# Optimization experiments

Hardware: AMD Instinct MI355X
Metric: run time of the kernel (lower is better)

Reference implementation:

```python
import jax, jax.numpy as jnp
import numpy as np

D, H, W, C = 24, 24, 16, 2        # image_dims + num_classes
THETA_ALPHA = 160.0               # bilateral spatial std
THETA_BETA = 3.0                  # bilateral intensity std
THETA_GAMMA = 3.0                 # spatial-only std
NUM_ITERATIONS = 5
N = D * H * W


def _gauss_kernel(feats):
    # Dense Gaussian kernel K_ij = exp(-0.5 * ||f_i - f_j||^2).
    # This is the exact filter that the permutohedral lattice approximates
    # (self-term included, matching the lattice splat/blur/slice behaviour).
    sq = jnp.sum(feats * feats, axis=-1)               # [N]
    d2 = sq[:, None] + sq[None, :] - 2.0 * feats @ feats.T
    return jnp.exp(-0.5 * jnp.maximum(d2, 0.0))        # [N, N]


def _positions():
    zz, yy, xx = jnp.meshgrid(jnp.arange(D), jnp.arange(H), jnp.arange(W), indexing='ij')
    return jnp.stack([zz, yy, xx], axis=-1).reshape(N, 3).astype(jnp.float32)


def setup_inputs() -> dict:
    key = jax.random.key(0)
    k1, k2 = jax.random.split(key)
    unaries = jax.random.normal(k1, (1, D, H, W, C), dtype=jnp.float32)
    rgb = jax.random.uniform(k2, (1, D, H, W, 1), dtype=jnp.float32)
    # learned params (build() initial values)
    spatial_ker_weights = jnp.array([1.41, 1.41], dtype=jnp.float32)
    bilateral_ker_weights = jnp.array([3.85, 3.85], dtype=jnp.float32)
    compatibility_matrix = jnp.eye(C, dtype=jnp.float32)
    return dict(unaries=unaries, rgb=rgb,
                spatial_ker_weights=spatial_ker_weights,
                bilateral_ker_weights=bilateral_ker_weights,
                compatibility_matrix=compatibility_matrix)


def reference(unaries, rgb, spatial_ker_weights, bilateral_ker_weights, compatibility_matrix):
    out_shape = unaries.shape
    u = unaries.reshape(N, C)                 # batch index 0 only, as in the TF code
    img = rgb.reshape(N, -1)
    pos = _positions()

    Ks = _gauss_kernel(pos / THETA_GAMMA)                                        # spatial kernel [N,N]
    Kb = _gauss_kernel(jnp.concatenate([pos / THETA_ALPHA, img / THETA_BETA], -1))  # bilateral kernel [N,N]

    # normalization = filter applied to all-ones (row sums)
    norm_s = jnp.sum(Ks, axis=-1, keepdims=True)   # [N,1]
    norm_b = jnp.sum(Kb, axis=-1, keepdims=True)   # [N,1]

    q = u
    for _ in range(NUM_ITERATIONS):
        spatial_out = (Ks @ q) / norm_s            # [N,C]
        bilateral_out = (Kb @ q) / norm_b          # [N,C]
        # diag(w_s) @ spatial.T + diag(w_b) @ bilateral.T  ==  per-class scaling
        message = spatial_out * spatial_ker_weights + bilateral_out * bilateral_ker_weights
        pairwise = message @ compatibility_matrix.T  # (compat @ msg.T).T
        q = u - pairwise
    return q.reshape(out_shape)
```

## Files before the change

kernel.cpp:

```cpp
#include <hip/hip_runtime.h>


#define DD 24
#define HH 24
#define WW 16
#define SLICE 384
#define NPTS 9216
#define NT 5
#define NPAIR 6
#define NPTOT 9
#define LOG2E 1.4426950408889634f
#define K3L   (LOG2E / 18.0f)
#define K160L (LOG2E / 51200.0f)
#define EXP2  __builtin_amdgcn_exp2f

static __device__ __forceinline__ int iabs(int a) { return a < 0 ? -a : a; }

__global__ __launch_bounds__(SLICE)
void k_pre(const float2* __restrict__ u2, const float* __restrict__ rgb,
           float2* __restrict__ tmp2, float* __restrict__ normS) {
    __shared__ float gk[32];
    __shared__ float2 sA[HH][WW + 1];
    __shared__ float2 sB[HH][WW + 1];
    const int z = blockIdx.x, p = blockIdx.y, t = threadIdx.x;
    const int y = t >> 4, x = t & 15;
    const int i = z * SLICE + t;

    const float kk = (p == 0) ? K3L : K160L;
    if (t < DD) gk[t] = EXP2(-(float)(t * t) * kk);

    const float I3 = rgb[i] * (1.f / 3.f);
    float Pt[NT];
    Pt[0] = EXP2(-0.5f * LOG2E * I3 * I3);
#pragma unroll
    for (int k = 1; k < NT; ++k) Pt[k] = Pt[k - 1] * I3;

    float2 v;
    if (p == 0) {
        v = u2[i];
    } else if (p < NPAIR) {
        float2 q = u2[i];
        float P = Pt[p - 1];
        v = make_float2(P * q.x, P * q.y);
    } else {
        int j = p - NPAIR;
        v = make_float2(Pt[2 * j], (j < 2) ? Pt[2 * j + 1] : 0.f);
    }
    sA[y][x] = v;
    __syncthreads();

    float a0 = 0.f, a1 = 0.f;
#pragma unroll
    for (int xp = 0; xp < WW; ++xp) {
        float w = gk[iabs(x - xp)];
        float2 vv = sA[y][xp];
        a0 = fmaf(w, vv.x, a0);
        a1 = fmaf(w, vv.y, a1);
    }
    sB[y][x] = make_float2(a0, a1);
    __syncthreads();
    float b0 = 0.f, b1 = 0.f;
#pragma unroll
    for (int yp = 0; yp < HH; ++yp) {
        float w = gk[iabs(y - yp)];
        float2 vv = sB[yp][x];
        b0 = fmaf(w, vv.x, b0);
        b1 = fmaf(w, vv.y, b1);
    }
    tmp2[p * NPTS + i] = make_float2(b0, b1);

    if (p == 0) {
        float sx = 0.f, sy = 0.f, sz = 0.f;
#pragma unroll
        for (int xp = 0; xp < WW; ++xp) sx += gk[iabs(x - xp)];
#pragma unroll
        for (int yp = 0; yp < HH; ++yp) sy += gk[iabs(y - yp)];
#pragma unroll
        for (int zp = 0; zp < DD; ++zp) sz += gk[iabs(z - zp)];
        normS[i] = 1.0f / (sx * sy * sz);
    }
}

__global__ __launch_bounds__(SLICE)
void k_zconv(const float2* __restrict__ tmp2, float2* __restrict__ zout2) {
    const int z = blockIdx.x, p = blockIdx.y, t = threadIdx.x;
    const float kk = (p == 0) ? K3L : K160L;
    float acc0 = 0.f, acc1 = 0.f;
    const float2* src = tmp2 + p * NPTS + t;
#pragma unroll 6
    for (int zp = 0; zp < DD; ++zp) {
        int d = z - zp;
        float w = EXP2(-(float)(d * d) * kk);
        float2 v = src[zp * SLICE];
        acc0 = fmaf(w, v.x, acc0);
        acc1 = fmaf(w, v.y, acc1);
    }
    zout2[p * NPTS + z * SLICE + t] = make_float2(acc0, acc1);
}

static __device__ __forceinline__ void mf_update(
        const float2 zp_[NPAIR], const float* Pt, float inv_ns, float inv_nb,
        const float* sw, const float* bw, const float* compat,
        const float2 uu, float* q0o, float* q1o) {
    const float invf[NT] = {1.f, 1.f, 0.5f, 1.f / 6.f, 1.f / 24.f};
    float b0 = 0.f, b1 = 0.f;
#pragma unroll
    for (int k = 0; k < NT; ++k) {
        float w = Pt[k] * invf[k];
        b0 = fmaf(w, zp_[1 + k].x, b0);
        b1 = fmaf(w, zp_[1 + k].y, b1);
    }
    b0 *= inv_nb;
    b1 *= inv_nb;
    float s0 = zp_[0].x * inv_ns;
    float s1 = zp_[0].y * inv_ns;
    float m0 = s0 * sw[0] + b0 * bw[0];
    float m1 = s1 * sw[1] + b1 * bw[1];
    float p0 = fmaf(compat[0], m0, compat[1] * m1);
    float p1 = fmaf(compat[2], m0, compat[3] * m1);
    *q0o = uu.x - p0;
    *q1o = uu.y - p1;
}

__global__ __launch_bounds__(SLICE)
void k_xyupd(const float2* __restrict__ zout2, const float* __restrict__ rgb,
             const float2* __restrict__ u2,
             const float* __restrict__ sw, const float* __restrict__ bw,
             const float* __restrict__ compat,
             const float* __restrict__ normS, float* __restrict__ normB,
             float2* __restrict__ tmp2, int it) {
    __shared__ float gk[32];
    __shared__ float2 sA[HH][WW + 1];
    __shared__ float2 sB[HH][WW + 1];
    const int z = blockIdx.x, p = blockIdx.y, t = threadIdx.x;
    const int y = t >> 4, x = t & 15;
    const int i = z * SLICE + t;

    const float kk = (p == 0) ? K3L : K160L;
    if (t < DD) gk[t] = EXP2(-(float)(t * t) * kk);

    float2 zp_[NPAIR];
#pragma unroll
    for (int k = 0; k < NPAIR; ++k) zp_[k] = zout2[k * NPTS + i];

    const float I3 = rgb[i] * (1.f / 3.f);
    float Pt[NT];
    Pt[0] = EXP2(-0.5f * LOG2E * I3 * I3);
#pragma unroll
    for (int k = 1; k < NT; ++k) Pt[k] = Pt[k - 1] * I3;

    float inv_nb;
    if (it == 0) {
        float2 n0 = zout2[6 * NPTS + i];
        float2 n1 = zout2[7 * NPTS + i];
        float2 n2 = zout2[8 * NPTS + i];
        float nb = Pt[0] * n0.x + Pt[1] * n0.y + 0.5f * Pt[2] * n1.x
                 + (1.f / 6.f) * Pt[3] * n1.y + (1.f / 24.f) * Pt[4] * n2.x;
        if (p == 0) normB[i] = nb;
        inv_nb = 1.0f / nb;
    } else {
        inv_nb = 1.0f / normB[i];
    }

    float q0, q1;
    mf_update(zp_, Pt, normS[i], inv_nb, sw, bw, compat, u2[i], &q0, &q1);

    float2 v;
    if (p == 0) v = make_float2(q0, q1);
    else { float P = Pt[p - 1]; v = make_float2(P * q0, P * q1); }

    sA[y][x] = v;
    __syncthreads();
    float a0 = 0.f, a1 = 0.f;
#pragma unroll
    for (int xp = 0; xp < WW; ++xp) {
        float w = gk[iabs(x - xp)];
        float2 vv = sA[y][xp];
        a0 = fmaf(w, vv.x, a0);
        a1 = fmaf(w, vv.y, a1);
    }
    sB[y][x] = make_float2(a0, a1);
    __syncthreads();
    float b0 = 0.f, b1 = 0.f;
#pragma unroll
    for (int yp = 0; yp < HH; ++yp) {
        float w = gk[iabs(y - yp)];
        float2 vv = sB[yp][x];
        b0 = fmaf(w, vv.x, b0);
        b1 = fmaf(w, vv.y, b1);
    }
    tmp2[p * NPTS + i] = make_float2(b0, b1);
}

__global__ __launch_bounds__(256)
void k_final(const float2* __restrict__ zout2, const float* __restrict__ rgb,
             const float2* __restrict__ u2,
             const float* __restrict__ sw, const float* __restrict__ bw,
             const float* __restrict__ compat,
             const float* __restrict__ normS, const float* __restrict__ normB,
             float2* __restrict__ out) {
    const int i = blockIdx.x * 256 + threadIdx.x;

    float2 zp_[NPAIR];
#pragma unroll
    for (int k = 0; k < NPAIR; ++k) zp_[k] = zout2[k * NPTS + i];

    const float I3 = rgb[i] * (1.f / 3.f);
    float Pt[NT];
    Pt[0] = EXP2(-0.5f * LOG2E * I3 * I3);
#pragma unroll
    for (int k = 1; k < NT; ++k) Pt[k] = Pt[k - 1] * I3;

    float q0, q1;
    mf_update(zp_, Pt, normS[i], 1.0f / normB[i], sw, bw, compat,
              u2[i], &q0, &q1);
    out[i] = make_float2(q0, q1);
}

extern "C" void kernel_launch(void* const* d_in, const int* in_sizes, int n_in,
                              void* d_out, int out_size, void* d_ws, size_t ws_size,
                              hipStream_t stream) {
    const float2* u2     = (const float2*)d_in[0];
    const float*  rgb    = (const float*)d_in[1];
    const float*  sw     = (const float*)d_in[2];
    const float*  bw     = (const float*)d_in[3];
    const float*  compat = (const float*)d_in[4];
    float2* out = (float2*)d_out;

    float2* ws2   = (float2*)d_ws;
    float2* tmp2  = ws2;
    float2* zout2 = ws2 + NPTOT * NPTS;
    float*  normS = (float*)(ws2 + 2 * NPTOT * NPTS);
    float*  normB = normS + NPTS;

    k_pre<<<dim3(DD, NPTOT), SLICE, 0, stream>>>(u2, rgb, tmp2, normS);

    for (int it = 0; it < 5; ++it) {
        k_zconv<<<dim3(DD, it == 0 ? NPTOT : NPAIR), SLICE, 0, stream>>>(tmp2, zout2);
        if (it < 4)
            k_xyupd<<<dim3(DD, NPAIR), SLICE, 0, stream>>>(zout2, rgb, u2, sw, bw,
                                                           compat, normS, normB,
                                                           tmp2, it);
        else
            k_final<<<NPTS / 256, 256, 0, stream>>>(zout2, rgb, u2, sw, bw,
                                                    compat, normS, normB, out);
    }
}
```

Measured before the change: 97.98 us.

## Fuse full 3D separable convolution per channel into one block with atomic message accumulation

Each of the pairing channels is now processed by a single 512-thread block that holds the whole 24x24x16 volume in LDS and runs the x, y and z passes in place, replacing the separate xy and z kernels. The mean-field update is split so that each channel block atomically adds its weighted contribution into a per-iteration message buffer, which the next iteration or the final kernel reads. This cuts the kernel launch count and global round trips. The cost is that only 6-9 blocks run on a GPU with many CUs, the two float components are filtered in sequence, and float atomics make the summation order nondeterministic.

```diff
diff --git a/kernel.cpp b/kernel.cpp
--- a/kernel.cpp
+++ b/kernel.cpp
@@ -4,217 +4,308 @@
 #define DD 24
 #define HH 24
 #define WW 16
-#define SLICE 384
+#define XS 17
+#define YSTR (HH * XS)
 #define NPTS 9216
+#define NBLK 512
+#define PPT 18
 #define NT 5
-#define NPAIR 6
-#define NPTOT 9
 #define LOG2E 1.4426950408889634f
 #define K3L   (LOG2E / 18.0f)
 #define K160L (LOG2E / 51200.0f)
 #define EXP2  __builtin_amdgcn_exp2f
 
-static __device__ __forceinline__ int iabs(int a) { return a < 0 ? -a : a; }
-
-__global__ __launch_bounds__(SLICE)
+#define LIDX(i) (XS * ((i) >> 4) + ((i) & 15))
+
+static __device__ __forceinline__ void pass_x(float* A, const float* w, int t) {
+    float i0[WW], o0[WW], i1[WW], o1[WW];
+    const int b0 = XS * t;
+    const int b1 = XS * (NBLK + t);
+    const bool two = (t < (DD * HH - NBLK));
+#pragma unroll
+    for (int xp = 0; xp < WW; ++xp) i0[xp] = A[b0 + xp];
+    if (two) {
+#pragma unroll
+        for (int xp = 0; xp < WW; ++xp) i1[xp] = A[b1 + xp];
+    }
+#pragma unroll
+    for (int x = 0; x < WW; ++x) {
+        float a = 0.f;
+#pragma unroll
+        for (int xp = 0; xp < WW; ++xp)
+            a = fmaf(w[x > xp ? x - xp : xp - x], i0[xp], a);
+        o0[x] = a;
+    }
+    if (two) {
+#pragma unroll
+        for (int x = 0; x < WW; ++x) {
+            float a = 0.f;
+#pragma unroll
+            for (int xp = 0; xp < WW; ++xp)
+                a = fmaf(w[x > xp ? x - xp : xp - x], i1[xp], a);
+            o1[x] = a;
+        }
+    }
+    __syncthreads();
+#pragma unroll
+    for (int x = 0; x < WW; ++x) A[b0 + x] = o0[x];
+    if (two) {
+#pragma unroll
+        for (int x = 0; x < WW; ++x) A[b1 + x] = o1[x];
+    }
+    __syncthreads();
+}
+
+static __device__ __forceinline__ void pass_y(float* A, const float* w, int t) {
+    float in[HH], o[HH];
+    const bool act = (t < DD * WW);
+    const int base = (t >> 4) * YSTR + (t & 15);
+    if (act) {
+#pragma unroll
+        for (int yp = 0; yp < HH; ++yp) in[yp] = A[base + XS * yp];
+#pragma unroll
+        for (int y = 0; y < HH; ++y) {
+            float a = 0.f;
+#pragma unroll
+            for (int yp = 0; yp < HH; ++yp)
+                a = fmaf(w[y > yp ? y - yp : yp - y], in[yp], a);
+            o[y] = a;
+        }
+    }
+    __syncthreads();
+    if (act) {
+#pragma unroll
+        for (int y = 0; y < HH; ++y) A[base + XS * y] = o[y];
+    }
+    __syncthreads();
+}
+
+static __device__ __forceinline__ void pass_z(float* A, const float* w, int t) {
+    float in[DD], o[DD];
+    const bool act = (t < HH * WW);
+    const int base = (t >> 4) * XS + (t & 15);
+    if (act) {
+#pragma unroll
+        for (int zp = 0; zp < DD; ++zp) in[zp] = A[base + YSTR * zp];
+#pragma unroll
+        for (int z = 0; z < DD; ++z) {
+            float a = 0.f;
+#pragma unroll
+            for (int zp = 0; zp < DD; ++zp)
+                a = fmaf(w[z > zp ? z - zp : zp - z], in[zp], a);
+            o[z] = a;
+        }
+    }
+    __syncthreads();
+    if (act) {
+#pragma unroll
+        for (int z = 0; z < DD; ++z) A[base + YSTR * z] = o[z];
+    }
+    __syncthreads();
+}
+
+static __device__ __forceinline__ void conv3(float* A, const float* w, int t) {
+    pass_x(A, w, t);
+    pass_y(A, w, t);
+    pass_z(A, w, t);
+}
+
+__global__ __launch_bounds__(NBLK, 2)
 void k_pre(const float2* __restrict__ u2, const float* __restrict__ rgb,
-           float2* __restrict__ tmp2, float* __restrict__ normS) {
-    __shared__ float gk[32];
-    __shared__ float2 sA[HH][WW + 1];
-    __shared__ float2 sB[HH][WW + 1];
-    const int z = blockIdx.x, p = blockIdx.y, t = threadIdx.x;
-    const int y = t >> 4, x = t & 15;
-    const int i = z * SLICE + t;
-
+           float2* __restrict__ zout, float* __restrict__ normS,
+           float2* __restrict__ msgAll) {
+    __shared__ float A[DD * YSTR];
+    __shared__ float sxl[WW], syl[HH], szl[DD];
+    const int p = blockIdx.x, t = threadIdx.x;
     const float kk = (p == 0) ? K3L : K160L;
-    if (t < DD) gk[t] = EXP2(-(float)(t * t) * kk);
-
-    const float I3 = rgb[i] * (1.f / 3.f);
-    float Pt[NT];
-    Pt[0] = EXP2(-0.5f * LOG2E * I3 * I3);
-#pragma unroll
-    for (int k = 1; k < NT; ++k) Pt[k] = Pt[k - 1] * I3;
-
-    float2 v;
+
+    float w[24];
+#pragma unroll
+    for (int d = 0; d < 24; ++d) w[d] = EXP2(-(float)(d * d) * kk);
+
+    {
+        int g = p * NBLK + t;
+        for (int j = g; j < 4 * NPTS; j += 9 * NBLK)
+            msgAll[j] = make_float2(0.f, 0.f);
+    }
+
     if (p == 0) {
-        v = u2[i];
-    } else if (p < NPAIR) {
-        float2 q = u2[i];
-        float P = Pt[p - 1];
-        v = make_float2(P * q.x, P * q.y);
-    } else {
-        int j = p - NPAIR;
-        v = make_float2(Pt[2 * j], (j < 2) ? Pt[2 * j + 1] : 0.f);
-    }
-    sA[y][x] = v;
-    __syncthreads();
-
-    float a0 = 0.f, a1 = 0.f;
-#pragma unroll
-    for (int xp = 0; xp < WW; ++xp) {
-        float w = gk[iabs(x - xp)];
-        float2 vv = sA[y][xp];
-        a0 = fmaf(w, vv.x, a0);
-        a1 = fmaf(w, vv.y, a1);
-    }
-    sB[y][x] = make_float2(a0, a1);
-    __syncthreads();
-    float b0 = 0.f, b1 = 0.f;
-#pragma unroll
-    for (int yp = 0; yp < HH; ++yp) {
-        float w = gk[iabs(y - yp)];
-        float2 vv = sB[yp][x];
-        b0 = fmaf(w, vv.x, b0);
-        b1 = fmaf(w, vv.y, b1);
-    }
-    tmp2[p * NPTS + i] = make_float2(b0, b1);
+        if (t < WW) {
+            float s = 0.f;
+            for (int xp = 0; xp < WW; ++xp) {
+                float d = (float)(t - xp);
+                s += EXP2(-d * d * K3L);
+            }
+            sxl[t] = s;
+        } else if (t >= 64 && t < 64 + HH) {
+            int y = t - 64; float s = 0.f;
+            for (int yp = 0; yp < HH; ++yp) {
+                float d = (float)(y - yp);
+                s += EXP2(-d * d * K3L);
+            }
+            syl[y] = s;
+        } else if (t >= 128 && t < 128 + DD) {
+            int z = t - 128; float s = 0.f;
+            for (int zp = 0; zp < DD; ++zp) {
+                float d = (float)(z - zp);
+                s += EXP2(-d * d * K3L);
+            }
+            szl[z] = s;
+        }
+    }
+
+    float vy[PPT], f0[PPT];
+#pragma unroll
+    for (int k = 0; k < PPT; ++k) {
+        const int i = t + k * NBLK;
+        float2 v;
+        if (p == 0) {
+            v = u2[i];
+        } else {
+            const float I3 = rgb[i] * (1.f / 3.f);
+            const float Pt0 = EXP2(-0.5f * LOG2E * I3 * I3);
+            const float Pt1 = Pt0 * I3, Pt2 = Pt1 * I3, Pt3 = Pt2 * I3,
+                        Pt4 = Pt3 * I3;
+            if (p < 6) {
+                const float P = (p == 1) ? Pt0 : (p == 2) ? Pt1 :
+                                (p == 3) ? Pt2 : (p == 4) ? Pt3 : Pt4;
+                float2 q = u2[i];
+                v = make_float2(P * q.x, P * q.y);
+            } else {
+                const int j = p - 6;
+                v = make_float2((j == 0) ? Pt0 : (j == 1) ? Pt2 : Pt4,
+                                (j == 0) ? Pt1 : (j == 1) ? Pt3 : 0.f);
+            }
+        }
+        A[LIDX(i)] = v.x;
+        vy[k] = v.y;
+    }
+    __syncthreads();
 
     if (p == 0) {
-        float sx = 0.f, sy = 0.f, sz = 0.f;
-#pragma unroll
-        for (int xp = 0; xp < WW; ++xp) sx += gk[iabs(x - xp)];
-#pragma unroll
-        for (int yp = 0; yp < HH; ++yp) sy += gk[iabs(y - yp)];
-#pragma unroll
-        for (int zp = 0; zp < DD; ++zp) sz += gk[iabs(z - zp)];
-        normS[i] = 1.0f / (sx * sy * sz);
-    }
-}
-
-__global__ __launch_bounds__(SLICE)
-void k_zconv(const float2* __restrict__ tmp2, float2* __restrict__ zout2) {
-    const int z = blockIdx.x, p = blockIdx.y, t = threadIdx.x;
+#pragma unroll
+        for (int k = 0; k < PPT; ++k) {
+            const int i = t + k * NBLK;
+            const int x = i & 15, rowid = i >> 4;
+            const int y = rowid % HH, z = rowid / HH;
+            normS[i] = 1.f / (sxl[x] * syl[y] * szl[z]);
+        }
+    }
+
+    conv3(A, w, t);
+#pragma unroll
+    for (int k = 0; k < PPT; ++k) f0[k] = A[LIDX(t + k * NBLK)];
+    __syncthreads();
+#pragma unroll
+    for (int k = 0; k < PPT; ++k) A[LIDX(t + k * NBLK)] = vy[k];
+    __syncthreads();
+    conv3(A, w, t);
+
+#pragma unroll
+    for (int k = 0; k < PPT; ++k) {
+        const int i = t + k * NBLK;
+        zout[p * NPTS + i] = make_float2(f0[k], A[LIDX(i)]);
+    }
+}
+
+__global__ __launch_bounds__(NBLK, 2)
+void k_fused(const float2* __restrict__ zout, const float2* __restrict__ msgPrev,
+             float2* __restrict__ msgNext, const float* __restrict__ rgb,
+             const float2* __restrict__ u2, const float* __restrict__ sw,
+             const float* __restrict__ bw, const float* __restrict__ compat,
+             const float* __restrict__ normS, float* __restrict__ normB,
+             int it) {
+    __shared__ float A[DD * YSTR];
+    const int p = blockIdx.x, t = threadIdx.x;
     const float kk = (p == 0) ? K3L : K160L;
-    float acc0 = 0.f, acc1 = 0.f;
-    const float2* src = tmp2 + p * NPTS + t;
-#pragma unroll 6
-    for (int zp = 0; zp < DD; ++zp) {
-        int d = z - zp;
-        float w = EXP2(-(float)(d * d) * kk);
-        float2 v = src[zp * SLICE];
-        acc0 = fmaf(w, v.x, acc0);
-        acc1 = fmaf(w, v.y, acc1);
-    }
-    zout2[p * NPTS + z * SLICE + t] = make_float2(acc0, acc1);
-}
-
-static __device__ __forceinline__ void mf_update(
-        const float2 zp_[NPAIR], const float* Pt, float inv_ns, float inv_nb,
-        const float* sw, const float* bw, const float* compat,
-        const float2 uu, float* q0o, float* q1o) {
-    const float invf[NT] = {1.f, 1.f, 0.5f, 1.f / 6.f, 1.f / 24.f};
-    float b0 = 0.f, b1 = 0.f;
-#pragma unroll
-    for (int k = 0; k < NT; ++k) {
-        float w = Pt[k] * invf[k];
-        b0 = fmaf(w, zp_[1 + k].x, b0);
-        b1 = fmaf(w, zp_[1 + k].y, b1);
-    }
-    b0 *= inv_nb;
-    b1 *= inv_nb;
-    float s0 = zp_[0].x * inv_ns;
-    float s1 = zp_[0].y * inv_ns;
-    float m0 = s0 * sw[0] + b0 * bw[0];
-    float m1 = s1 * sw[1] + b1 * bw[1];
-    float p0 = fmaf(compat[0], m0, compat[1] * m1);
-    float p1 = fmaf(compat[2], m0, compat[3] * m1);
-    *q0o = uu.x - p0;
-    *q1o = uu.y - p1;
-}
-
-__global__ __launch_bounds__(SLICE)
-void k_xyupd(const float2* __restrict__ zout2, const float* __restrict__ rgb,
-             const float2* __restrict__ u2,
-             const float* __restrict__ sw, const float* __restrict__ bw,
-             const float* __restrict__ compat,
-             const float* __restrict__ normS, float* __restrict__ normB,
-             float2* __restrict__ tmp2, int it) {
-    __shared__ float gk[32];
-    __shared__ float2 sA[HH][WW + 1];
-    __shared__ float2 sB[HH][WW + 1];
-    const int z = blockIdx.x, p = blockIdx.y, t = threadIdx.x;
-    const int y = t >> 4, x = t & 15;
-    const int i = z * SLICE + t;
-
-    const float kk = (p == 0) ? K3L : K160L;
-    if (t < DD) gk[t] = EXP2(-(float)(t * t) * kk);
-
-    float2 zp_[NPAIR];
-#pragma unroll
-    for (int k = 0; k < NPAIR; ++k) zp_[k] = zout2[k * NPTS + i];
-
-    const float I3 = rgb[i] * (1.f / 3.f);
-    float Pt[NT];
-    Pt[0] = EXP2(-0.5f * LOG2E * I3 * I3);
-#pragma unroll
-    for (int k = 1; k < NT; ++k) Pt[k] = Pt[k - 1] * I3;
-
-    float inv_nb;
-    if (it == 0) {
-        float2 n0 = zout2[6 * NPTS + i];
-        float2 n1 = zout2[7 * NPTS + i];
-        float2 n2 = zout2[8 * NPTS + i];
-        float nb = Pt[0] * n0.x + Pt[1] * n0.y + 0.5f * Pt[2] * n1.x
-                 + (1.f / 6.f) * Pt[3] * n1.y + (1.f / 24.f) * Pt[4] * n2.x;
-        if (p == 0) normB[i] = nb;
-        inv_nb = 1.0f / nb;
-    } else {
-        inv_nb = 1.0f / normB[i];
-    }
-
-    float q0, q1;
-    mf_update(zp_, Pt, normS[i], inv_nb, sw, bw, compat, u2[i], &q0, &q1);
-
-    float2 v;
-    if (p == 0) v = make_float2(q0, q1);
-    else { float P = Pt[p - 1]; v = make_float2(P * q0, P * q1); }
-
-    sA[y][x] = v;
-    __syncthreads();
-    float a0 = 0.f, a1 = 0.f;
-#pragma unroll
-    for (int xp = 0; xp < WW; ++xp) {
-        float w = gk[iabs(x - xp)];
-        float2 vv = sA[y][xp];
-        a0 = fmaf(w, vv.x, a0);
-        a1 = fmaf(w, vv.y, a1);
-    }
-    sB[y][x] = make_float2(a0, a1);
-    __syncthreads();
-    float b0 = 0.f, b1 = 0.f;
-#pragma unroll
-    for (int yp = 0; yp < HH; ++yp) {
-        float w = gk[iabs(y - yp)];
-        float2 vv = sB[yp][x];
-        b0 = fmaf(w, vv.x, b0);
-        b1 = fmaf(w, vv.y, b1);
-    }
-    tmp2[p * NPTS + i] = make_float2(b0, b1);
+
+    float w[24];
+#pragma unroll
+    for (int d = 0; d < 24; ++d) w[d] = EXP2(-(float)(d * d) * kk);
+
+    const float c00 = compat[0], c01 = compat[1], c10 = compat[2], c11 = compat[3];
+    const float sw0 = sw[0], sw1 = sw[1], bw0 = bw[0], bw1 = bw[1];
+
+    float vy[PPT], cc[PPT], f0[PPT];
+#pragma unroll
+    for (int k = 0; k < PPT; ++k) {
+        const int i = t + k * NBLK;
+        const float I3 = rgb[i] * (1.f / 3.f);
+        const float Pt0 = EXP2(-0.5f * LOG2E * I3 * I3);
+        const float Pt1 = Pt0 * I3, Pt2 = Pt1 * I3, Pt3 = Pt2 * I3,
+                    Pt4 = Pt3 * I3;
+        float q0, q1, ccv;
+        if (it == 1) {
+            float2 zs  = zout[i];
+            float2 zb0 = zout[1 * NPTS + i], zb1 = zout[2 * NPTS + i];
+            float2 zb2 = zout[3 * NPTS + i], zb3 = zout[4 * NPTS + i];
+            float2 zb4 = zout[5 * NPTS + i];
+            float2 n0  = zout[6 * NPTS + i], n1 = zout[7 * NPTS + i];
+            float2 n2  = zout[8 * NPTS + i];
+            const float nb = Pt0 * n0.x + Pt1 * n0.y + 0.5f * Pt2 * n1.x
+                           + (1.f / 6.f) * Pt3 * n1.y + (1.f / 24.f) * Pt4 * n2.x;
+            if (p == 0) normB[i] = nb;
+            const float inv_nb = 1.f / nb;
+            const float inv_ns = normS[i];
+            float b0 = Pt0 * zb0.x + Pt1 * zb1.x + 0.5f * Pt2 * zb2.x
+                     + (1.f / 6.f) * Pt3 * zb3.x + (1.f / 24.f) * Pt4 * zb4.x;
+            float b1 = Pt0 * zb0.y + Pt1 * zb1.y + 0.5f * Pt2 * zb2.y
+                     + (1.f / 6.f) * Pt3 * zb3.y + (1.f / 24.f) * Pt4 * zb4.y;
+            b0 *= inv_nb; b1 *= inv_nb;
+            const float s0 = zs.x * inv_ns, s1 = zs.y * inv_ns;
+            const float m0 = s0 * sw0 + b0 * bw0;
+            const float m1 = s1 * sw1 + b1 * bw1;
+            const float2 uu = u2[i];
+            q0 = uu.x - (c00 * m0 + c01 * m1);
+            q1 = uu.y - (c10 * m0 + c11 * m1);
+            ccv = (p == 0) ? inv_ns : inv_nb;
+        } else {
+            const float2 m = msgPrev[i];
+            const float2 uu = u2[i];
+            q0 = uu.x - (c00 * m.x + c01 * m.y);
+            q1 = uu.y - (c10 * m.x + c11 * m.y);
+            ccv = (p == 0) ? normS[i] : (1.f / normB[i]);
+        }
+        if (p == 0) {
+            A[LIDX(i)] = q0; vy[k] = q1; cc[k] = ccv;
+        } else {
+            const float P = (p == 1) ? Pt0 : (p == 2) ? Pt1 :
+                            (p == 3) ? Pt2 : (p == 4) ? Pt3 : Pt4;
+            const float invfp = (p <= 2) ? 1.f : (p == 3) ? 0.5f :
+                                (p == 4) ? (1.f / 6.f) : (1.f / 24.f);
+            A[LIDX(i)] = P * q0; vy[k] = P * q1; cc[k] = ccv * P * invfp;
+        }
+    }
+    __syncthreads();
+
+    conv3(A, w, t);
+#pragma unroll
+    for (int k = 0; k < PPT; ++k) f0[k] = A[LIDX(t + k * NBLK)];
+    __syncthreads();
+#pragma unroll
+    for (int k = 0; k < PPT; ++k) A[LIDX(t + k * NBLK)] = vy[k];
+    __syncthreads();
+    conv3(A, w, t);
+
+    const float cw0 = (p == 0) ? sw0 : bw0;
+    const float cw1 = (p == 0) ? sw1 : bw1;
+#pragma unroll
+    for (int k = 0; k < PPT; ++k) {
+        const int i = t + k * NBLK;
+        unsafeAtomicAdd(&msgNext[i].x, cc[k] * cw0 * f0[k]);
+        unsafeAtomicAdd(&msgNext[i].y, cc[k] * cw1 * A[LIDX(i)]);
+    }
 }
 
 __global__ __launch_bounds__(256)
-void k_final(const float2* __restrict__ zout2, const float* __restrict__ rgb,
-             const float2* __restrict__ u2,
-             const float* __restrict__ sw, const float* __restrict__ bw,
-             const float* __restrict__ compat,
-             const float* __restrict__ normS, const float* __restrict__ normB,
-             float2* __restrict__ out) {
+void k_final(const float2* __restrict__ msg, const float2* __restrict__ u2,
+             const float* __restrict__ compat, float2* __restrict__ out) {
     const int i = blockIdx.x * 256 + threadIdx.x;
-
-    float2 zp_[NPAIR];
-#pragma unroll
-    for (int k = 0; k < NPAIR; ++k) zp_[k] = zout2[k * NPTS + i];
-
-    const float I3 = rgb[i] * (1.f / 3.f);
-    float Pt[NT];
-    Pt[0] = EXP2(-0.5f * LOG2E * I3 * I3);
-#pragma unroll
-    for (int k = 1; k < NT; ++k) Pt[k] = Pt[k - 1] * I3;
-
-    float q0, q1;
-    mf_update(zp_, Pt, normS[i], 1.0f / normB[i], sw, bw, compat,
-              u2[i], &q0, &q1);
-    out[i] = make_float2(q0, q1);
+    const float c00 = compat[0], c01 = compat[1], c10 = compat[2], c11 = compat[3];
+    const float2 m = msg[i];
+    const float2 uu = u2[i];
+    out[i] = make_float2(uu.x - (c00 * m.x + c01 * m.y),
+                         uu.y - (c10 * m.x + c11 * m.y));
 }
 
 extern "C" void kernel_launch(void* const* d_in, const int* in_sizes, int n_in,
@@ -227,22 +318,20 @@
     const float*  compat = (const float*)d_in[4];
     float2* out = (float2*)d_out;
 
-    float2* ws2   = (float2*)d_ws;
-    float2* tmp2  = ws2;
-    float2* zout2 = ws2 + NPTOT * NPTS;
-    float*  normS = (float*)(ws2 + 2 * NPTOT * NPTS);
-    float*  normB = normS + NPTS;
-
-    k_pre<<<dim3(DD, NPTOT), SLICE, 0, stream>>>(u2, rgb, tmp2, normS);
-
-    for (int it = 0; it < 5; ++it) {
-        k_zconv<<<dim3(DD, it == 0 ? NPTOT : NPAIR), SLICE, 0, stream>>>(tmp2, zout2);
-        if (it < 4)
-            k_xyupd<<<dim3(DD, NPAIR), SLICE, 0, stream>>>(zout2, rgb, u2, sw, bw,
-                                                           compat, normS, normB,
-                                                           tmp2, it);
-        else
-            k_final<<<NPTS / 256, 256, 0, stream>>>(zout2, rgb, u2, sw, bw,
-                                                    compat, normS, normB, out);
-    }
-}
+    float2* ws2    = (float2*)d_ws;
+    float2* zout   = ws2;
+    float2* msgAll = ws2 + 9 * NPTS;
+    float*  normS  = (float*)(ws2 + 13 * NPTS);
+    float*  normB  = normS + NPTS;
+
+    k_pre<<<9, NBLK, 0, stream>>>(u2, rgb, zout, normS, msgAll);
+    for (int it = 1; it <= 4; ++it) {
+        const float2* mprev = (it >= 2) ? (msgAll + (size_t)(it - 2) * NPTS)
+                                        : msgAll;
+        k_fused<<<6, NBLK, 0, stream>>>(zout, mprev,
+                                        msgAll + (size_t)(it - 1) * NPTS,
+                                        rgb, u2, sw, bw, compat,
+                                        normS, normB, it);
+    }
+    k_final<<<NPTS / 256, 256, 0, stream>>>(msgAll + 3 * NPTS, u2, compat, out);
+}
```

Result: slower. 209.0 us (+113.3%).
